# Kernel optimization log

Measured on AMD Instinct MI355X. Metric: run time of the kernel, lower is better.

The kernel has to match this reference:

```python
import jax, jax.numpy as jnp
import numpy as np

# Topology constants (size='medium')
N_SW = 131      # 49 + 32 + 24 + 16 + 10
N_L = 64        # n_wavelengths
N_M = 32        # n_modes
PS = 4          # patch_size
V1_START, V1_COUNT = 0, 49
OUT_START, OUT_COUNT = 121, 10
DECAY = 0.15


def _encode(images):
    # images: [B, 28, 28] -> patches [B, 49, 16] -> pad to n_modes -> [B, 49, 64, 32]
    B = images.shape[0]
    p = images[:, :28, :28].reshape(B, 7, PS, 7, PS)
    p = p.transpose(0, 1, 3, 2, 4).reshape(B, 49, PS * PS)
    p = jnp.pad(p, ((0, 0), (0, 0), (0, N_M - PS * PS)))
    w_idx = jnp.arange(N_L, dtype=jnp.float32)
    w_weights = 1.0 - jnp.abs(w_idx - 32.0) / 64.0
    return p[:, :, None, :] * w_weights[None, None, :, None]


def _phase_step(field_r, field_i, out_r, out_i, conn_r, conn_i, phase, gain_sp):
    # Complex gather over switch graph: contract source switch dim s against conn[s, t]
    g_r = jnp.einsum('bsLm,st->btLm', out_r, conn_r) - jnp.einsum('bsLm,st->btLm', out_i, conn_i)
    g_i = jnp.einsum('bsLm,st->btLm', out_r, conn_i) + jnp.einsum('bsLm,st->btLm', out_i, conn_r)
    cp = jnp.cos(phase)[None, :, None, None]
    sp = jnp.sin(phase)[None, :, None, None]
    gr = g_r * cp - g_i * sp
    gi = g_r * sp + g_i * cp
    field_r = field_r * (1.0 - DECAY) + gr * 0.25
    field_i = field_i * (1.0 - DECAY) + gi * 0.25
    mag = jnp.sqrt(field_r ** 2 + field_i ** 2 + 1e-8)
    new_mag = jnp.tanh(mag * gain_sp[None, :, None, None])
    scale = new_mag / (mag + 1e-8)
    return field_r, field_i, field_r * scale, field_i * scale


def setup_inputs() -> dict:
    key = jax.random.key(0)
    k_img, k_mag, k_ph, k_w = jax.random.split(key, 4)
    images = jax.random.normal(k_img, (128, 28, 28), dtype=jnp.float32)
    conn_mag = jnp.abs(jax.random.normal(k_mag, (N_SW, N_SW), dtype=jnp.float32)) * 0.03
    conn_phase = jax.random.normal(k_ph, (N_SW, N_SW), dtype=jnp.float32) * 0.1
    conn_real = conn_mag * jnp.cos(conn_phase)
    conn_imag = conn_mag * jnp.sin(conn_phase)
    switch_phase = jnp.zeros((N_SW,), dtype=jnp.float32)
    switch_gain = jnp.ones((N_SW,), dtype=jnp.float32)
    readout_w = jax.random.normal(k_w, (10, OUT_COUNT), dtype=jnp.float32) * 0.1
    readout_b = jnp.zeros((10,), dtype=jnp.float32)
    return {
        'images': images,
        'conn_real': conn_real,
        'conn_imag': conn_imag,
        'switch_phase': switch_phase,
        'switch_gain': switch_gain,
        'readout_w': readout_w,
        'readout_b': readout_b,
        'n_steps': 10,
        'injection_steps': 4,
    }


def reference(images, conn_real, conn_imag, switch_phase, switch_gain,
              readout_w, readout_b, n_steps, injection_steps):
    enc = _encode(images)
    enc_max = jnp.max(jnp.abs(enc))
    enc = enc * jnp.where(enc_max > 1e-8, 1.0 / enc_max, 1.0)
    B = images.shape[0]
    field_r = jnp.zeros((B, N_SW, N_L, N_M), dtype=images.dtype)
    field_i = jnp.zeros_like(field_r)
    out_r = jnp.zeros_like(field_r)
    out_i = jnp.zeros_like(field_r)
    gain_sp = jax.nn.softplus(switch_gain)
    inj = enc * 0.3  # [B, 49, 64, 32], goes into V1 slots
    for t in range(n_steps):
        if t < injection_steps:
            field_r = field_r.at[:, V1_START:V1_START + V1_COUNT].add(inj)
        field_r, field_i, out_r, out_i = _phase_step(
            field_r, field_i, out_r, out_i, conn_real, conn_imag, switch_phase, gain_sp)
    orr = out_r[:, OUT_START:OUT_START + OUT_COUNT]
    oii = out_i[:, OUT_START:OUT_START + OUT_COUNT]
    energy = (orr ** 2 + oii ** 2).sum(axis=(2, 3))
    features = jnp.log1p(energy + 1e-8)
    return features @ readout_w.T + readout_b
```

## Files before the change

kernel.cpp:

```cpp
#include <hip/hip_runtime.h>
#include <cmath>


#define NSTEPS  10
#define INJ_ST  4
#define MT      144
#define NTASK   4224

typedef __bf16 bf16x8 __attribute__((ext_vector_type(8)));
typedef __bf16 bf16x4 __attribute__((ext_vector_type(4)));
typedef short  short8 __attribute__((ext_vector_type(8)));
typedef float  f32x4  __attribute__((ext_vector_type(4)));

#define WS_MAX    0
#define WS_ENERGY 64
#define WS_GSP    2048
#define WS_CONN   4096

__global__ void k_pre(const float* __restrict__ img,
                      const float* __restrict__ cr, const float* __restrict__ ci,
                      const float* __restrict__ phase, const float* __restrict__ gain,
                      float* ws) {
    if (blockIdx.x < 98) {
        __shared__ float sm[256];
        float v = 0.f;
        for (int i = blockIdx.x * 256 + threadIdx.x; i < 128 * 28 * 28; i += 98 * 256)
            v = fmaxf(v, fabsf(img[i]));
        sm[threadIdx.x] = v;
        __syncthreads();
        for (int s = 128; s > 0; s >>= 1) {
            if (threadIdx.x < s) sm[threadIdx.x] = fmaxf(sm[threadIdx.x], sm[threadIdx.x + s]);
            __syncthreads();
        }
        if (threadIdx.x == 0)
            atomicMax((unsigned int*)(ws + WS_MAX), __float_as_uint(sm[0]));
        return;
    }
    int i = (blockIdx.x - 98) * 256 + threadIdx.x;
    __bf16* Cb = (__bf16*)(ws + WS_CONN);
    const int NCE = MT * 160;
    if (i < NCE) {
        int m = i / 160, k = i % 160;
        float vr = 0.f, vi = 0.f;
        if (m < 131 && k < 131) {
            float a = cr[k * 131 + m], b = ci[k * 131 + m];
            float ph = phase[m];
            float cp = cosf(ph), sp = sinf(ph);
            vr = a * cp - b * sp;
            vi = a * sp + b * cp;
        }
        int ca = ((k >> 3) * MT + m) * 8 + (k & 7);
        Cb[ca]       = (__bf16)vr;
        Cb[NCE + ca] = (__bf16)vi;
    } else if (i < NCE + MT) {
        int j = i - NCE;
        float g = 0.f;
        if (j < 131) {
            float x = gain[j];
            g = (x > 20.f) ? x : log1pf(expf(x));
        }
        ws[WS_GSP + j] = g * -0.72134754543f;
    }
}

static __device__ __forceinline__ f32x4 MF(bf16x8 a, bf16x8 b, f32x4 c) {
    return __builtin_amdgcn_mfma_f32_16x16x32_bf16(a, b, c, 0, 0, 0);
}
static __device__ __forceinline__ bf16x8 bneg(bf16x8 a) {
    short8 t = __builtin_bit_cast(short8, a) ^ (short8)(short)0x8000;
    return __builtin_bit_cast(bf16x8, t);
}

#define CPAIR(AR, AI, BR, BI, BNI, P)                                  \
    accr[P] = MF(AR, BR,  accr[P]);                                    \
    accr[P] = MF(AI, BNI, accr[P]);                                    \
    acci[P] = MF(AR, BI,  acci[P]);                                    \
    acci[P] = MF(AI, BR,  acci[P]);

__global__ __launch_bounds__(512, 2)
void k_main(const float* __restrict__ img, const float* __restrict__ ws,
            float* __restrict__ energy) {
    __shared__ __bf16 CrL[18 * MT * 8];
    __shared__ __bf16 CiL[18 * MT * 8];
    __shared__ __bf16 OBP[2][8][18 * 16 * 8];
    __shared__ float  gspL[144];

    const int tid  = threadIdx.x;
    const int lane = tid & 63;
    const int ln15 = lane & 15;
    const int quad = lane >> 4;
    const int w    = __builtin_amdgcn_readfirstlane(tid >> 6);

    __bf16* __restrict__ OWr = &OBP[0][w][0];
    __bf16* __restrict__ OWi = &OBP[1][w][0];

    const float mx = ws[WS_MAX];
    const float sc = (mx > 1e-8f) ? (1.02f / mx) : 1.02f;

    {
        const int4* srcR = (const int4*)(ws + WS_CONN);
        const int4* srcI = (const int4*)(ws + WS_CONN + (MT * 160 / 2));
        int4* dstR = (int4*)CrL;
        int4* dstI = (int4*)CiL;
        for (int i = tid; i < 2592; i += 512) { dstR[i] = srcR[i]; dstI[i] = srcI[i]; }
        if (tid < 144) gspL[tid] = ws[WS_GSP + tid];
    }
    __syncthreads();

#pragma unroll 1
    for (int r = 0; r < 3; ++r) {
        int T;
        if (r < 2) {
            T = r * 2048 + blockIdx.x * 8 + w;
        } else {
            if (w != 0 || blockIdx.x >= 128) break;
            T = 4096 + blockIdx.x;
        }
        if (T >= NTASK) break;
        const int u  = T >> 7;
        const int im = T & 127;
        const float wl  = 1.0f - fabsf((float)u - 32.0f) * (1.0f / 64.0f);
        const float wgt = (u == 0 || u == 32) ? 1.0f : 2.0f;
        const int imgb = im * 784 + (ln15 >> 2) * 28 + (ln15 & 3);

        f32x4 accr[9], acci[9];
#pragma unroll
        for (int p = 0; p < 9; ++p) { accr[p] = (f32x4)0.f; acci[p] = (f32x4)0.f; }

        auto inj_add = [&]() {
#pragma unroll
            for (int mt = 0; mt < 4; ++mt) {
#pragma unroll
                for (int rr = 0; rr < 4; ++rr) {
                    int j = mt * 16 + quad * 4 + rr;
                    if (j < 49) {
                        int pi = j / 7, pj = j % 7;
                        float px = img[imgb + pi * 112 + pj * 4];
                        float t  = px * sc;
                        accr[mt][rr] = fmaf(t, wl, accr[mt][rr]);
                    }
                }
            }
        };

        auto epilogue = [&]() {
#pragma unroll
            for (int mt = 0; mt < 9; ++mt) {
                f32x4 g2v = *(const f32x4*)(gspL + mt * 16 + quad * 4);
                bf16x4 pr, pi;
#pragma unroll
                for (int rr = 0; rr < 4; ++rr) {
                    float ar = accr[mt][rr], ai = acci[mt][rr];
                    float mag2 = fmaf(ar, ar, fmaf(ai, ai, 1.6e-7f));
                    float rsq  = __builtin_amdgcn_rsqf(mag2);
                    float e    = __builtin_amdgcn_exp2f(g2v[rr] * (mag2 * rsq));
                    float uu   = __builtin_amdgcn_rcpf(1.0f + e);
                    float th   = fmaf(-2.0f, e * uu, 1.0f);
                    float scv  = th * rsq;
                    pr[rr] = (__bf16)(ar * scv); pi[rr] = (__bf16)(ai * scv);
                }
                const int off = ((mt * 2 + (quad >> 1)) * 16 + ln15) * 8
                              + (quad & 1) * 4;
                *(bf16x4*)(OWr + off) = pr;
                *(bf16x4*)(OWi + off) = pi;
            }
        };

        inj_add();
        epilogue();

#pragma unroll 1
        for (int t = 1; t < NSTEPS - 1; ++t) {
#pragma unroll
            for (int p = 0; p < 9; ++p) { accr[p] *= 0.85f; acci[p] *= 0.85f; }
            if (t < INJ_ST) inj_add();

            const int ktEnd = (t == 1) ? 2 : 5;
#pragma unroll 1
            for (int kt = 0; kt < ktEnd; ++kt) {
                const int kch = kt * 4 + quad;
                const int rk  = (kch > 17) ? 17 : kch;
                const int bb  = (rk * 16 + ln15) * 8;
                bf16x8 br = *(const bf16x8*)(OWr + bb);
                bf16x8 bi = *(const bf16x8*)(OWi + bb);
                const int ab = (rk * MT + ln15) * 8;
                bf16x8 ar[9], ai[9];
#pragma unroll
                for (int mt = 0; mt < 9; ++mt) {
                    ar[mt] = *(const bf16x8*)(CrL + ab + mt * 128);
                    ai[mt] = *(const bf16x8*)(CiL + ab + mt * 128);
                }
                bf16x8 bn = bneg(bi);
#pragma unroll
                for (int mt = 0; mt < 9; ++mt) {
                    CPAIR(ar[mt], ai[mt], br, bi, bn, mt)
                }
            }
            epilogue();
        }

        accr[7] *= 0.85f; acci[7] *= 0.85f;
        accr[8] *= 0.85f; acci[8] *= 0.85f;
#pragma unroll 1
        for (int kt = 0; kt < 5; ++kt) {
            const int kch = kt * 4 + quad;
            const int rk  = (kch > 17) ? 17 : kch;
            const int bb  = (rk * 16 + ln15) * 8;
            bf16x8 br = *(const bf16x8*)(OWr + bb);
            bf16x8 bi = *(const bf16x8*)(OWi + bb);
            const int ab = (rk * MT + ln15) * 8;
            bf16x8 ar7 = *(const bf16x8*)(CrL + ab + 7 * 128);
            bf16x8 ai7 = *(const bf16x8*)(CiL + ab + 7 * 128);
            bf16x8 ar8 = *(const bf16x8*)(CrL + ab + 8 * 128);
            bf16x8 ai8 = *(const bf16x8*)(CiL + ab + 8 * 128);
            bf16x8 bn = bneg(bi);
            CPAIR(ar7, ai7, br, bi, bn, 7)
            CPAIR(ar8, ai8, br, bi, bn, 8)
        }

#pragma unroll
        for (int mt = 7; mt < 9; ++mt) {
#pragma unroll
            for (int rr = 0; rr < 4; ++rr) {
                int j = mt * 16 + quad * 4 + rr;
                if (j >= 121 && j <= 130) {
                    float ar = accr[mt][rr], ai = acci[mt][rr];
                    float mag2 = fmaf(ar, ar, fmaf(ai, ai, 1.6e-7f));
                    float rsq  = __builtin_amdgcn_rsqf(mag2);
                    float e    = __builtin_amdgcn_exp2f(gspL[j] * (mag2 * rsq));
                    float uu   = __builtin_amdgcn_rcpf(1.0f + e);
                    float th   = fmaf(-2.0f, e * uu, 1.0f);
                    float scv  = th * rsq;
                    float orv = ar * scv, oiv = ai * scv;
                    float e2 = orv * orv + oiv * oiv;
                    e2 += __shfl_xor(e2, 1);
                    e2 += __shfl_xor(e2, 2);
                    e2 += __shfl_xor(e2, 4);
                    e2 += __shfl_xor(e2, 8);
                    if (ln15 == 0)
                        atomicAdd(energy + im * 10 + (j - 121), e2 * wgt);
                }
            }
        }
    }
}

__global__ void k_readout(const float* __restrict__ ws,
                          const float* __restrict__ W,
                          const float* __restrict__ bias,
                          float* __restrict__ out) {
    int i = blockIdx.x * 256 + threadIdx.x;
    if (i < 1280) {
        int b = i / 10, o = i % 10;
        float s = bias[o];
#pragma unroll
        for (int f = 0; f < 10; ++f) {
            float feat = log1pf(ws[WS_ENERGY + b * 10 + f] + 1e-8f);
            s = fmaf(feat, W[o * 10 + f], s);
        }
        out[i] = s;
    }
}

extern "C" void kernel_launch(void* const* d_in, const int* in_sizes, int n_in,
                              void* d_out, int out_size, void* d_ws, size_t ws_size,
                              hipStream_t stream) {
    const float* images = (const float*)d_in[0];
    const float* conn_r = (const float*)d_in[1];
    const float* conn_i = (const float*)d_in[2];
    const float* phase  = (const float*)d_in[3];
    const float* gain   = (const float*)d_in[4];
    const float* W      = (const float*)d_in[5];
    const float* bias   = (const float*)d_in[6];
    float* ws  = (float*)d_ws;
    float* out = (float*)d_out;

    hipMemsetAsync(ws, 0, (WS_ENERGY + 1280) * sizeof(float), stream);
    hipLaunchKernelGGL(k_pre, dim3(189), dim3(256), 0, stream,
                       images, conn_r, conn_i, phase, gain, ws);
    hipLaunchKernelGGL(k_main, dim3(256), dim3(512), 0, stream,
                       images, ws, ws + WS_ENERGY);
    hipLaunchKernelGGL(k_readout, dim3(5), dim3(256), 0, stream, ws, W, bias, out);
}
```

Baseline: 188.3 us.

## Fuse preprocessing, main loop and readout into one cooperative kernel

Replaces the memset plus three launches (pre, main, readout) with a single cooperative-launch kernel that uses grid-wide syncs. Each block rebuilds the rotated bf16 connection matrix straight into LDS and computes its own partial image max. The global max is reduced after a grid sync, and a second grid sync precedes the in-kernel readout. This removes launch gaps and the workspace round-trip, but every block now redoes the connection preprocessing and pays for two grid barriers.

```diff
diff --git a/kernel.cpp b/kernel.cpp
--- a/kernel.cpp
+++ b/kernel.cpp
@@ -1,5 +1,8 @@
 #include <hip/hip_runtime.h>
+#include <hip/hip_cooperative_groups.h>
 #include <cmath>
+
+namespace cg = cooperative_groups;
 
 
 #define NSTEPS  10
@@ -12,56 +15,8 @@
 typedef short  short8 __attribute__((ext_vector_type(8)));
 typedef float  f32x4  __attribute__((ext_vector_type(4)));
 
-#define WS_MAX    0
 #define WS_ENERGY 64
-#define WS_GSP    2048
-#define WS_CONN   4096
-
-__global__ void k_pre(const float* __restrict__ img,
-                      const float* __restrict__ cr, const float* __restrict__ ci,
-                      const float* __restrict__ phase, const float* __restrict__ gain,
-                      float* ws) {
-    if (blockIdx.x < 98) {
-        __shared__ float sm[256];
-        float v = 0.f;
-        for (int i = blockIdx.x * 256 + threadIdx.x; i < 128 * 28 * 28; i += 98 * 256)
-            v = fmaxf(v, fabsf(img[i]));
-        sm[threadIdx.x] = v;
-        __syncthreads();
-        for (int s = 128; s > 0; s >>= 1) {
-            if (threadIdx.x < s) sm[threadIdx.x] = fmaxf(sm[threadIdx.x], sm[threadIdx.x + s]);
-            __syncthreads();
-        }
-        if (threadIdx.x == 0)
-            atomicMax((unsigned int*)(ws + WS_MAX), __float_as_uint(sm[0]));
-        return;
-    }
-    int i = (blockIdx.x - 98) * 256 + threadIdx.x;
-    __bf16* Cb = (__bf16*)(ws + WS_CONN);
-    const int NCE = MT * 160;
-    if (i < NCE) {
-        int m = i / 160, k = i % 160;
-        float vr = 0.f, vi = 0.f;
-        if (m < 131 && k < 131) {
-            float a = cr[k * 131 + m], b = ci[k * 131 + m];
-            float ph = phase[m];
-            float cp = cosf(ph), sp = sinf(ph);
-            vr = a * cp - b * sp;
-            vi = a * sp + b * cp;
-        }
-        int ca = ((k >> 3) * MT + m) * 8 + (k & 7);
-        Cb[ca]       = (__bf16)vr;
-        Cb[NCE + ca] = (__bf16)vi;
-    } else if (i < NCE + MT) {
-        int j = i - NCE;
-        float g = 0.f;
-        if (j < 131) {
-            float x = gain[j];
-            g = (x > 20.f) ? x : log1pf(expf(x));
-        }
-        ws[WS_GSP + j] = g * -0.72134754543f;
-    }
-}
+#define WS_PMAX   1536
 
 static __device__ __forceinline__ f32x4 MF(bf16x8 a, bf16x8 b, f32x4 c) {
     return __builtin_amdgcn_mfma_f32_16x16x32_bf16(a, b, c, 0, 0, 0);
@@ -78,12 +33,17 @@
     acci[P] = MF(AI, BR,  acci[P]);
 
 __global__ __launch_bounds__(512, 2)
-void k_main(const float* __restrict__ img, const float* __restrict__ ws,
-            float* __restrict__ energy) {
+void k_all(const float* __restrict__ img,
+           const float* __restrict__ cr, const float* __restrict__ ci,
+           const float* __restrict__ phase, const float* __restrict__ gain,
+           const float* __restrict__ W, const float* __restrict__ bias,
+           float* __restrict__ ws, float* __restrict__ out) {
     __shared__ __bf16 CrL[18 * MT * 8];
     __shared__ __bf16 CiL[18 * MT * 8];
     __shared__ __bf16 OBP[2][8][18 * 16 * 8];
     __shared__ float  gspL[144];
+    __shared__ float  wmax[8];
+    __shared__ float  scratch[264];
 
     const int tid  = threadIdx.x;
     const int lane = tid & 63;
@@ -93,19 +53,67 @@
 
     __bf16* __restrict__ OWr = &OBP[0][w][0];
     __bf16* __restrict__ OWi = &OBP[1][w][0];
-
-    const float mx = ws[WS_MAX];
+    float*  __restrict__ energy = ws + WS_ENERGY;
+
+    {
+        float v = 0.f;
+        for (int i = blockIdx.x * 512 + tid; i < 128 * 28 * 28; i += 256 * 512)
+            v = fmaxf(v, fabsf(img[i]));
+#pragma unroll
+        for (int off = 32; off > 0; off >>= 1)
+            v = fmaxf(v, __shfl_xor(v, off));
+        if (lane == 0) wmax[w] = v;
+    }
+    if (tid < 131) {
+        float ph = phase[tid];
+        scratch[tid]       = cosf(ph);
+        scratch[132 + tid] = sinf(ph);
+    }
+    if (tid < 144) {
+        float g = 0.f;
+        if (tid < 131) {
+            float x = gain[tid];
+            g = (x > 20.f) ? x : log1pf(expf(x));
+        }
+        gspL[tid] = g * -0.72134754543f;
+    }
+    if (blockIdx.x == 0)
+        for (int i = tid; i < 1280; i += 512) ws[WS_ENERGY + i] = 0.f;
+    __syncthreads();
+    if (tid == 0) {
+        float bm = wmax[0];
+#pragma unroll
+        for (int q = 1; q < 8; ++q) bm = fmaxf(bm, wmax[q]);
+        __hip_atomic_store(ws + WS_PMAX + blockIdx.x, bm,
+                           __ATOMIC_RELAXED, __HIP_MEMORY_SCOPE_AGENT);
+    }
+    for (int i = tid; i < 18 * MT * 8; i += 512) {
+        int ch = i / (MT * 8), rem = i % (MT * 8);
+        int m = rem >> 3, kl = rem & 7, k = ch * 8 + kl;
+        float vr = 0.f, vi = 0.f;
+        if (m < 131 && k < 131) {
+            float a = cr[k * 131 + m], b = ci[k * 131 + m];
+            float cp = scratch[m], sp = scratch[132 + m];
+            vr = a * cp - b * sp;
+            vi = a * sp + b * cp;
+        }
+        CrL[i] = (__bf16)vr;
+        CiL[i] = (__bf16)vi;
+    }
+
+    cg::this_grid().sync();
+    __syncthreads();
+
+    if (tid < 256)
+        scratch[tid] = __hip_atomic_load(ws + WS_PMAX + tid,
+                                         __ATOMIC_RELAXED, __HIP_MEMORY_SCOPE_AGENT);
+    __syncthreads();
+    for (int s = 128; s > 0; s >>= 1) {
+        if (tid < s) scratch[tid] = fmaxf(scratch[tid], scratch[tid + s]);
+        __syncthreads();
+    }
+    const float mx = scratch[0];
     const float sc = (mx > 1e-8f) ? (1.02f / mx) : 1.02f;
-
-    {
-        const int4* srcR = (const int4*)(ws + WS_CONN);
-        const int4* srcI = (const int4*)(ws + WS_CONN + (MT * 160 / 2));
-        int4* dstR = (int4*)CrL;
-        int4* dstI = (int4*)CiL;
-        for (int i = tid; i < 2592; i += 512) { dstR[i] = srcR[i]; dstI[i] = srcI[i]; }
-        if (tid < 144) gspL[tid] = ws[WS_GSP + tid];
-    }
-    __syncthreads();
 
 #pragma unroll 1
     for (int r = 0; r < 3; ++r) {
@@ -243,22 +251,20 @@
             }
         }
     }
-}
-
-__global__ void k_readout(const float* __restrict__ ws,
-                          const float* __restrict__ W,
-                          const float* __restrict__ bias,
-                          float* __restrict__ out) {
-    int i = blockIdx.x * 256 + threadIdx.x;
-    if (i < 1280) {
-        int b = i / 10, o = i % 10;
+
+    cg::this_grid().sync();
+    const int oi = blockIdx.x * 512 + tid;
+    if (oi < 1280) {
+        int b = oi / 10, o = oi % 10;
         float s = bias[o];
 #pragma unroll
         for (int f = 0; f < 10; ++f) {
-            float feat = log1pf(ws[WS_ENERGY + b * 10 + f] + 1e-8f);
+            float ev = __hip_atomic_load(ws + WS_ENERGY + b * 10 + f,
+                                         __ATOMIC_RELAXED, __HIP_MEMORY_SCOPE_AGENT);
+            float feat = log1pf(ev + 1e-8f);
             s = fmaf(feat, W[o * 10 + f], s);
         }
-        out[i] = s;
+        out[oi] = s;
     }
 }
 
@@ -275,10 +281,9 @@
     float* ws  = (float*)d_ws;
     float* out = (float*)d_out;
 
-    hipMemsetAsync(ws, 0, (WS_ENERGY + 1280) * sizeof(float), stream);
-    hipLaunchKernelGGL(k_pre, dim3(189), dim3(256), 0, stream,
-                       images, conn_r, conn_i, phase, gain, ws);
-    hipLaunchKernelGGL(k_main, dim3(256), dim3(512), 0, stream,
-                       images, ws, ws + WS_ENERGY);
-    hipLaunchKernelGGL(k_readout, dim3(5), dim3(256), 0, stream, ws, W, bias, out);
-}
+    void* args[] = { (void*)&images, (void*)&conn_r, (void*)&conn_i,
+                     (void*)&phase, (void*)&gain, (void*)&W, (void*)&bias,
+                     (void*)&ws, (void*)&out };
+    hipLaunchCooperativeKernel((const void*)k_all, dim3(256), dim3(512),
+                               args, 0, stream);
+}
```

New measurement: 269.1 us. 42.9% more time.
